# Kernel tuning notes

Measured on AMD Instinct MI355X. Metric: run time of the kernel, lower is better.

Reference implementation:

```python
import jax, jax.numpy as jnp
import numpy as np

N, NFEAT, NHID, NCLASS, NHEAD = 8192, 512, 64, 16, 4
ALPHA = 0.1  # leaky relu slope
NEG = -9e15


def setup_inputs() -> dict:
    key = jax.random.key(0)
    ks = jax.random.split(key, 7)
    x = jax.random.normal(ks[0], (N, NFEAT), dtype=jnp.float32)
    adj = (jax.random.uniform(ks[1], (N, N)) < 0.05).astype(jnp.float32)
    # per-head params: W [H, nfeat, nhid], a [H, 2*nhid] (xavier-ish scale)
    W = jax.random.normal(ks[2], (NHEAD, NFEAT, NHID), dtype=jnp.float32) * (1.0 / np.sqrt(NFEAT))
    a = jax.random.normal(ks[3], (NHEAD, 2 * NHID), dtype=jnp.float32) * (1.0 / np.sqrt(NHID))
    W_out = jax.random.normal(ks[4], (NHEAD * NHID, NCLASS), dtype=jnp.float32) * (1.0 / np.sqrt(NHEAD * NHID))
    a_out = jax.random.normal(ks[5], (2 * NCLASS,), dtype=jnp.float32) * (1.0 / np.sqrt(NCLASS))
    return {"x": x, "adj": adj, "W": W, "a": a, "W_out": W_out, "a_out": a_out}


def _gat_layer(h, adj, Wk, ak):
    """Dense pyGAT GraphAttentionLayer (eval mode, dropout = identity)."""
    d = Wk.shape[1]
    Wh = h @ Wk                         # [N, d]
    f1 = Wh @ ak[:d]                    # [N]
    f2 = Wh @ ak[d:]                    # [N]
    e = jax.nn.leaky_relu(f1[:, None] + f2[None, :], negative_slope=ALPHA)  # [N, N]
    att = jax.nn.softmax(jnp.where(adj > 0, e, NEG), axis=1)
    return att @ Wh                     # [N, d]


def reference(x, adj, W, a, W_out, a_out):
    # eval mode: F.dropout is identity
    heads = jax.vmap(lambda Wk, ak: jax.nn.elu(_gat_layer(x, adj, Wk, ak)))(W, a)  # [H, N, nhid]
    h = jnp.transpose(heads, (1, 0, 2)).reshape(x.shape[0], -1)                    # [N, H*nhid]
    out = jax.nn.elu(_gat_layer(h, adj, W_out, a_out))                             # [N, nclass]
    return jax.nn.log_softmax(out, axis=1)
```

## Files before the change

### kernel.cpp

```cpp
#include <hip/hip_runtime.h>
#include <hip/hip_bf16.h>

#define NN 8192
#define NFEAT 512
#define NHID 64
#define NCLASS 16
#define NHEAD 4
#define ALPHA 0.1f
#define CAP 768
#define ZSPLIT 4
#define JPB (NN / ZSPLIT)
#define DCH 512

typedef short bf16x8 __attribute__((ext_vector_type(8)));
typedef float f32x4 __attribute__((ext_vector_type(4)));
typedef float fv4 __attribute__((ext_vector_type(4)));

__device__ __forceinline__ float lrelu(float x) { return fmaxf(x, ALPHA * x); }
__device__ __forceinline__ float elu(float x) { return x > 0.f ? x : __expf(x) - 1.f; }
__device__ __forceinline__ short f2b(float x) {
  union { __bf16 b; short s; } c; c.b = (__bf16)x; return c.s;
}
__device__ __forceinline__ float b2f(short x) {
  union { unsigned int u; float f; } c; c.u = ((unsigned int)(unsigned short)x) << 16; return c.f;
}

#define UPF(w, v, A0, A1)                                  \
  {                                                        \
    const float lo_ = __uint_as_float((v) << 16);          \
    const float hi_ = __uint_as_float((v) & 0xffff0000u);  \
    (A0) += (w) * lo_;                                     \
    (A1) += (w) * hi_;                                     \
  }

__global__ __launch_bounds__(256) void k_wprep(const float* __restrict__ W,
                                               short* __restrict__ WB) {
  __shared__ float t[64][65];
  const int h = blockIdx.y;
  const int k0 = blockIdx.x * 64;
  const int tid = threadIdx.x;
#pragma unroll
  for (int it = 0; it < 16; ++it) {
    const int r = it * 4 + (tid >> 6), c = tid & 63;
    t[r][c] = W[((size_t)h * NFEAT + k0 + r) * NHID + c];
  }
  __syncthreads();
#pragma unroll
  for (int it = 0; it < 16; ++it) {
    const int d = it * 4 + (tid >> 6), k = tid & 63;
    WB[((size_t)h * NHID + d) * NFEAT + k0 + k] = f2b(t[k][d]);
  }
}

__global__ __launch_bounds__(256) void k_prep1(const float* __restrict__ x,
                                               const short* __restrict__ WB,
                                               const float* __restrict__ a,
                                               short* __restrict__ Whf,
                                               float* __restrict__ f1i,
                                               float* __restrict__ f2i) {
  __shared__ short tile[64][72];
  const int bid = blockIdx.x;
  const int h = bid >> 7;
  const int bm = (bid & 127) * 64;
  const int tid = threadIdx.x;
  const int wv = tid >> 6, lane = tid & 63;
  const int mr = lane & 15, kg = lane >> 4;
  f32x4 acc0 = {0.f, 0.f, 0.f, 0.f}, acc1 = acc0, acc2 = acc0, acc3 = acc0;
  const float* ap = x + (size_t)(bm + wv * 16 + mr) * NFEAT + kg * 8;
  const short* bp = WB + ((size_t)h * NHID + mr) * NFEAT + kg * 8;
#pragma unroll 2
  for (int k0 = 0; k0 < NFEAT; k0 += 32) {
    const float4 xa = *reinterpret_cast<const float4*>(ap);
    const float4 xb = *reinterpret_cast<const float4*>(ap + 4);
    bf16x8 af;
    af[0] = f2b(xa.x); af[1] = f2b(xa.y); af[2] = f2b(xa.z); af[3] = f2b(xa.w);
    af[4] = f2b(xb.x); af[5] = f2b(xb.y); af[6] = f2b(xb.z); af[7] = f2b(xb.w);
    const bf16x8 b0 = *reinterpret_cast<const bf16x8*>(bp);
    const bf16x8 b1 = *reinterpret_cast<const bf16x8*>(bp + 16 * NFEAT);
    const bf16x8 b2 = *reinterpret_cast<const bf16x8*>(bp + 32 * NFEAT);
    const bf16x8 b3 = *reinterpret_cast<const bf16x8*>(bp + 48 * NFEAT);
    acc0 = __builtin_amdgcn_mfma_f32_16x16x32_bf16(af, b0, acc0, 0, 0, 0);
    acc1 = __builtin_amdgcn_mfma_f32_16x16x32_bf16(af, b1, acc1, 0, 0, 0);
    acc2 = __builtin_amdgcn_mfma_f32_16x16x32_bf16(af, b2, acc2, 0, 0, 0);
    acc3 = __builtin_amdgcn_mfma_f32_16x16x32_bf16(af, b3, acc3, 0, 0, 0);
    ap += 32; bp += 32;
  }
  float a1v[4], a2v[4];
#pragma unroll
  for (int c = 0; c < 4; ++c) {
    a1v[c] = a[h * 128 + mr + c * 16];
    a2v[c] = a[h * 128 + 64 + mr + c * 16];
  }
#pragma unroll
  for (int q = 0; q < 4; ++q) {
    float s1 = acc0[q] * a1v[0] + acc1[q] * a1v[1] + acc2[q] * a1v[2] + acc3[q] * a1v[3];
    float s2 = acc0[q] * a2v[0] + acc1[q] * a2v[1] + acc2[q] * a2v[2] + acc3[q] * a2v[3];
#pragma unroll
    for (int off = 1; off < 16; off <<= 1) {
      s1 += __shfl_xor(s1, off);
      s2 += __shfl_xor(s2, off);
    }
    if (mr == 0) {
      const int i = bm + wv * 16 + kg * 4 + q;
      f1i[(size_t)i * 4 + h] = s1;
      f2i[(size_t)i * 4 + h] = s2;
    }
  }
#pragma unroll
  for (int q = 0; q < 4; ++q) {
    const int r = wv * 16 + kg * 4 + q;
    tile[r][mr +  0] = f2b(acc0[q]);
    tile[r][mr + 16] = f2b(acc1[q]);
    tile[r][mr + 32] = f2b(acc2[q]);
    tile[r][mr + 48] = f2b(acc3[q]);
  }
  __syncthreads();
#pragma unroll
  for (int it = 0; it < 2; ++it) {
    const int jbl = (tid >> 6) + it * 4;
    const int d = tid & 63;
    bf16x8 o;
#pragma unroll
    for (int jo = 0; jo < 8; ++jo) o[jo] = tile[jbl * 8 + jo][d];
    *reinterpret_cast<bf16x8*>(Whf +
        (((size_t)h * 1024 + (bm >> 3) + jbl) * 64 + d) * 8) = o;
  }
}

__global__ __launch_bounds__(256) void k_rmax(const float* __restrict__ src,
                                              float* __restrict__ dst, int n, int stride,
                                              int boff) {
  const float* p = src + (size_t)blockIdx.x * boff;
  float m = -1e30f;
  for (int k = threadIdx.x; k < n; k += 256) m = fmaxf(m, p[(size_t)k * stride]);
#pragma unroll
  for (int off = 32; off; off >>= 1) m = fmaxf(m, __shfl_xor(m, off));
  __shared__ float sm[4];
  if ((threadIdx.x & 63) == 0) sm[threadIdx.x >> 6] = m;
  __syncthreads();
  if (threadIdx.x == 0) dst[blockIdx.x] = fmaxf(fmaxf(sm[0], sm[1]), fmaxf(sm[2], sm[3]));
}

__global__ __launch_bounds__(256) void k_acbd(const float* __restrict__ f1i,
                                              const float* __restrict__ f2i,
                                              const float* __restrict__ f2max,
                                              float2* __restrict__ ACh,
                                              unsigned int* __restrict__ BDh) {
  const int idx = blockIdx.x * 256 + threadIdx.x;
  const int i = idx & (NN - 1);
  const int h = idx >> 13;
  const float fm = f2max[h];
  const float f1 = f1i[(size_t)i * 4 + h];
  const float f2 = f2i[(size_t)i * 4 + h];
  const float s = f1 + fm;
  const float mrow = fmaxf(s, 0.1f * s);
  float2 ac;
  ac.x = __expf(s - mrow);
  ac.y = __expf(0.1f * s - mrow);
  ACh[(size_t)h * NN + i] = ac;
  const float t = f2 - fm;
  const unsigned int B = (unsigned short)f2b(__expf(t));
  const unsigned int D = (unsigned short)f2b(__expf(0.1f * t));
  BDh[(size_t)h * NN + i] = B | (D << 16);
}

__global__ __launch_bounds__(256) void k_scan(const float* __restrict__ adj,
                                              unsigned int* __restrict__ bmask) {
  const fv4* a4 = reinterpret_cast<const fv4*>(adj);
  const int t0 = blockIdx.x * 256 + threadIdx.x;
#pragma unroll 4
  for (int it = 0; it < 32; ++it) {
    const int g = it * 524288 + t0;
    const fv4 v = __builtin_nontemporal_load(a4 + g);
    unsigned int nv = (unsigned int)((v.x > 0.f) | ((v.y > 0.f) << 1) |
                                     ((v.z > 0.f) << 2) | ((v.w > 0.f) << 3))
                      << ((threadIdx.x & 7) * 4);
    nv |= __shfl_xor(nv, 1);
    nv |= __shfl_xor(nv, 2);
    nv |= __shfl_xor(nv, 4);
    if ((threadIdx.x & 7) == 0) bmask[g >> 3] = nv;
  }
}

__global__ __launch_bounds__(256) void k_dense1z(const unsigned int* __restrict__ bmask,
                                                 const short* __restrict__ Whf,
                                                 const float2* __restrict__ ACh,
                                                 const unsigned int* __restrict__ BDh,
                                                 float* __restrict__ OpP,
                                                 float* __restrict__ rsP) {
  __shared__ unsigned int sm_mask[64][16];
  __shared__ unsigned int sm_bd[DCH];
  const int i0 = blockIdx.x * 64;
  const int h = blockIdx.y;
  const int z = blockIdx.z;
  const int jb0 = z * JPB;
  const int tid = threadIdx.x;
  const int wv = tid >> 6, lane = tid & 63;
  const int mr = lane & 15, kg = lane >> 4;
  const int row_local = wv * 16 + mr;
  const float2 ac = ACh[(size_t)h * NN + i0 + row_local];
  f32x4 acc0 = {0.f, 0.f, 0.f, 0.f}, acc1 = acc0, acc2 = acc0, acc3 = acc0;
  float rs = 0.f;
  const int rr = tid >> 2, w0 = (tid & 3) * 4;

  for (int jc = jb0; jc < jb0 + JPB; jc += DCH) {
    __syncthreads();
    {
      const unsigned int* src = bmask + (size_t)(i0 + rr) * 256 + (jc >> 5);
#pragma unroll
      for (int u = 0; u < 4; ++u) sm_mask[rr][w0 + u] = src[w0 + u];
      sm_bd[tid] = BDh[(size_t)h * NN + jc + tid];
      sm_bd[tid + 256] = BDh[(size_t)h * NN + jc + tid + 256];
    }
    __syncthreads();
#pragma unroll 4
    for (int ks = 0; ks < DCH / 32; ++ks) {
      const int jl = ks * 32 + kg * 8;
      const uint4 bda = *reinterpret_cast<const uint4*>(&sm_bd[jl]);
      const uint4 bdb = *reinterpret_cast<const uint4*>(&sm_bd[jl + 4]);
      const unsigned int mb = (sm_mask[row_local][ks] >> (kg * 8)) & 0xffu;
      bf16x8 af;
#define MKW(e, bdw)                                              \
      {                                                          \
        const float Bf = __uint_as_float((bdw) << 16);           \
        const float Df = __uint_as_float((bdw) & 0xffff0000u);   \
        float w_ = fmaxf(ac.x * Bf, ac.y * Df);                  \
        w_ = ((mb >> (e)) & 1u) ? w_ : 0.f;                      \
        rs += w_;                                                \
        af[e] = f2b(w_);                                         \
      }
      MKW(0, bda.x) MKW(1, bda.y) MKW(2, bda.z) MKW(3, bda.w)
      MKW(4, bdb.x) MKW(5, bdb.y) MKW(6, bdb.z) MKW(7, bdb.w)
#undef MKW
      const short* wp = Whf + (((size_t)h * 1024 + ((jc + jl) >> 3)) * 64 + mr) * 8;
      const bf16x8 bf0 = *reinterpret_cast<const bf16x8*>(wp);
      const bf16x8 bf1 = *reinterpret_cast<const bf16x8*>(wp + 128);
      const bf16x8 bf2 = *reinterpret_cast<const bf16x8*>(wp + 256);
      const bf16x8 bf3 = *reinterpret_cast<const bf16x8*>(wp + 384);
      acc0 = __builtin_amdgcn_mfma_f32_16x16x32_bf16(af, bf0, acc0, 0, 0, 0);
      acc1 = __builtin_amdgcn_mfma_f32_16x16x32_bf16(af, bf1, acc1, 0, 0, 0);
      acc2 = __builtin_amdgcn_mfma_f32_16x16x32_bf16(af, bf2, acc2, 0, 0, 0);
      acc3 = __builtin_amdgcn_mfma_f32_16x16x32_bf16(af, bf3, acc3, 0, 0, 0);
    }
  }
  rs += __shfl_xor(rs, 16);
  rs += __shfl_xor(rs, 32);
  if (lane < 16)
    rsP[((size_t)z * NHEAD + h) * NN + i0 + wv * 16 + lane] = rs;
  float* op = OpP + (((size_t)z * NHEAD + h) * NN + i0) * 64;
#pragma unroll
  for (int q = 0; q < 4; ++q) {
    const int r = wv * 16 + kg * 4 + q;
    op[(size_t)r * 64 + mr +  0] = acc0[q];
    op[(size_t)r * 64 + mr + 16] = acc1[q];
    op[(size_t)r * 64 + mr + 32] = acc2[q];
    op[(size_t)r * 64 + mr + 48] = acc3[q];
  }
}

__global__ __launch_bounds__(256) void k_comb1(const float* __restrict__ OpP,
                                               const float* __restrict__ rsP,
                                               short* __restrict__ hcat) {
  const int idx = blockIdx.x * 256 + threadIdx.x;
  const int i = idx >> 8;
  const int hc = idx & 255;
  const int h = hc >> 6, d = hc & 63;
  float s = 0.f, rsum = 0.f;
#pragma unroll
  for (int z = 0; z < ZSPLIT; ++z) {
    s += OpP[(((size_t)z * NHEAD + h) * NN + i) * 64 + d];
    rsum += rsP[((size_t)z * NHEAD + h) * NN + i];
  }
  hcat[idx] = f2b(elu(s / rsum));
}

__global__ __launch_bounds__(256) void k_gemm2(const short* __restrict__ hcat,
                                               const float* __restrict__ Wout,
                                               const float* __restrict__ aout,
                                               short* __restrict__ Wh2B,
                                               float* __restrict__ f1o,
                                               float* __restrict__ f2o) {
  __shared__ float sW[NHEAD * NHID][NCLASS + 1];
  __shared__ float sh[16][NHEAD * NHID + 1];
  const int tid = threadIdx.x;
  const int r = tid >> 4, c = tid & 15;
  const int row = blockIdx.x * 16 + r;
  for (int u = tid; u < 256 * 16; u += 256) sW[u >> 4][u & 15] = Wout[u];
  for (int u = tid; u < 16 * 256; u += 256)
    sh[u >> 8][u & 255] = b2f(hcat[(size_t)(blockIdx.x * 16 + (u >> 8)) * 256 + (u & 255)]);
  __syncthreads();
  float acc = 0.f;
#pragma unroll 8
  for (int f = 0; f < 256; ++f) acc += sh[r][f] * sW[f][c];
  Wh2B[(size_t)row * NCLASS + c] = f2b(acc);
  float s1 = acc * aout[c];
  float s2 = acc * aout[NCLASS + c];
#pragma unroll
  for (int off = 8; off; off >>= 1) { s1 += __shfl_xor(s1, off); s2 += __shfl_xor(s2, off); }
  if (c == 0) { f1o[row] = s1; f2o[row] = s2; }
}

__global__ __launch_bounds__(256) void k_attn2(const unsigned int* __restrict__ bmask,
                                               const short* __restrict__ Wh2B,
                                               const float* __restrict__ f1o,
                                               const float* __restrict__ f2o,
                                               const float* __restrict__ f2omax,
                                               float* __restrict__ out) {
  __shared__ unsigned short idx[CAP];
  __shared__ unsigned int wj[CAP + 4];
  __shared__ float red[4][NCLASS];
  __shared__ float swp[4];
  __shared__ float sinvs;
  __shared__ int cnt;
  const int i = blockIdx.x;
  const int tid = threadIdx.x;
  const int wv = tid >> 6, lane = tid & 63;
  if (tid == 0) cnt = 0;
  __syncthreads();

  {
    unsigned int word = bmask[(size_t)i * 256 + tid];
    const int c = __popc(word);
    if (c) {
      int base = atomicAdd(&cnt, c);
      const int j0 = tid * 32;
      while (word) {
        const int b = __ffs(word) - 1;
        word &= word - 1;
        if (base < CAP) idx[base++] = (unsigned short)(j0 + b);
      }
    }
  }
  __syncthreads();
  const int n = min(cnt, CAP);
  if (tid < 4) wj[n + tid] = 0;

  const float f1r = f1o[i];
  const float mrow = lrelu(f1r + f2omax[0]);
  float sw = 0.f;
  for (int k = tid; k < n; k += 256) {
    const int j = idx[k];
    const float w = __expf(lrelu(f1r + f2o[j]) - mrow);
    wj[k] = ((unsigned int)(unsigned short)f2b(w) << 16) | (unsigned int)j;
    sw += w;
  }
#pragma unroll
  for (int off = 32; off; off >>= 1) sw += __shfl_xor(sw, off);
  if (lane == 0) swp[wv] = sw;
  __syncthreads();
  if (tid == 0) sinvs = 1.f / (swp[0] + swp[1] + swp[2] + swp[3]);
  __syncthreads();

  const int grp = tid >> 2, gl = tid & 3;
  float acc0 = 0.f, acc1 = 0.f, acc2 = 0.f, acc3 = 0.f;
  const short* wb = Wh2B + gl * 4;
  for (int kb = grp * 4; kb < n; kb += 256) {
    const uint4 pw = *reinterpret_cast<const uint4*>(wj + kb);
    const uint2 e0 = *reinterpret_cast<const uint2*>(wb + (size_t)(pw.x & 0xffffu) * NCLASS);
    const uint2 e1 = *reinterpret_cast<const uint2*>(wb + (size_t)(pw.y & 0xffffu) * NCLASS);
    const uint2 e2 = *reinterpret_cast<const uint2*>(wb + (size_t)(pw.z & 0xffffu) * NCLASS);
    const uint2 e3 = *reinterpret_cast<const uint2*>(wb + (size_t)(pw.w & 0xffffu) * NCLASS);
    const float w0 = __uint_as_float(pw.x & 0xffff0000u);
    const float w1 = __uint_as_float(pw.y & 0xffff0000u);
    const float w2 = __uint_as_float(pw.z & 0xffff0000u);
    const float w3 = __uint_as_float(pw.w & 0xffff0000u);
    UPF(w0, e0.x, acc0, acc1) UPF(w0, e0.y, acc2, acc3)
    UPF(w1, e1.x, acc0, acc1) UPF(w1, e1.y, acc2, acc3)
    UPF(w2, e2.x, acc0, acc1) UPF(w2, e2.y, acc2, acc3)
    UPF(w3, e3.x, acc0, acc1) UPF(w3, e3.y, acc2, acc3)
  }
  acc0 += __shfl_xor(acc0, 4);  acc1 += __shfl_xor(acc1, 4);
  acc2 += __shfl_xor(acc2, 4);  acc3 += __shfl_xor(acc3, 4);
  acc0 += __shfl_xor(acc0, 8);  acc1 += __shfl_xor(acc1, 8);
  acc2 += __shfl_xor(acc2, 8);  acc3 += __shfl_xor(acc3, 8);
  acc0 += __shfl_xor(acc0, 16); acc1 += __shfl_xor(acc1, 16);
  acc2 += __shfl_xor(acc2, 16); acc3 += __shfl_xor(acc3, 16);
  acc0 += __shfl_xor(acc0, 32); acc1 += __shfl_xor(acc1, 32);
  acc2 += __shfl_xor(acc2, 32); acc3 += __shfl_xor(acc3, 32);
  if (lane < 4) {
    red[wv][lane * 4 + 0] = acc0;
    red[wv][lane * 4 + 1] = acc1;
    red[wv][lane * 4 + 2] = acc2;
    red[wv][lane * 4 + 3] = acc3;
  }
  __syncthreads();
  if (tid < NCLASS) {
    const float s = red[0][tid] + red[1][tid] + red[2][tid] + red[3][tid];
    const float v = elu(s * sinvs);
    float vm = v;
#pragma unroll
    for (int off = 8; off; off >>= 1) vm = fmaxf(vm, __shfl_xor(vm, off, 16));
    float ex = __expf(v - vm);
#pragma unroll
    for (int off = 8; off; off >>= 1) ex += __shfl_xor(ex, off, 16);
    out[(size_t)i * NCLASS + tid] = v - vm - __logf(ex);
  }
}

extern "C" void kernel_launch(void* const* d_in, const int* in_sizes, int n_in,
                              void* d_out, int out_size, void* d_ws, size_t ws_size,
                              hipStream_t stream) {
  const float* x    = (const float*)d_in[0];
  const float* adj  = (const float*)d_in[1];
  const float* W    = (const float*)d_in[2];
  const float* a    = (const float*)d_in[3];
  const float* Wout = (const float*)d_in[4];
  const float* aout = (const float*)d_in[5];
  float* out = (float*)d_out;
  char* ws = (char*)d_ws;
  const size_t MB = 1048576;
  const size_t KB = 1024;

  unsigned int* bmask  = (unsigned int*)(ws);
  short* Whf           = (short*)(ws + 8 * MB);
  short* hcat          = (short*)(ws + 12 * MB);
  float* OpP           = (float*)(ws + 16 * MB);
  float* rsP           = (float*)(ws + 48 * MB);
  short* WB            = (short*)(ws + 49 * MB);
  float* f1i           = (float*)(ws + 49 * MB + 256 * KB);
  float* f2i           = (float*)(ws + 49 * MB + 384 * KB);
  float2* ACh          = (float2*)(ws + 49 * MB + 512 * KB);
  unsigned int* BDh    = (unsigned int*)(ws + 49 * MB + 768 * KB);
  float* f1o           = (float*)(ws + 49 * MB + 896 * KB);
  float* f2o           = (float*)(ws + 49 * MB + 928 * KB);
  short* Wh2B          = (short*)(ws + 49 * MB + 960 * KB);
  float* f2max         = (float*)(ws + 49 * MB + 1216 * KB);
  float* f2omax        = (float*)(ws + 49 * MB + 1216 * KB + 64);

  k_wprep<<<dim3(8, 4), 256, 0, stream>>>(W, WB);
  k_prep1<<<512, 256, 0, stream>>>(x, WB, a, Whf, f1i, f2i);
  k_rmax<<<NHEAD, 256, 0, stream>>>(f2i, f2max, NN, 4, 1);
  k_acbd<<<NN * NHEAD / 256, 256, 0, stream>>>(f1i, f2i, f2max, ACh, BDh);
  k_scan<<<2048, 256, 0, stream>>>(adj, bmask);
  k_dense1z<<<dim3(NN / 64, NHEAD, ZSPLIT), 256, 0, stream>>>(bmask, Whf, ACh, BDh, OpP, rsP);
  k_comb1<<<NN, 256, 0, stream>>>(OpP, rsP, hcat);
  k_gemm2<<<NN / 16, 256, 0, stream>>>(hcat, Wout, aout, Wh2B, f1o, f2o);
  k_rmax<<<1, 256, 0, stream>>>(f2o, f2omax, NN, 1, 0);
  k_attn2<<<NN, 256, 0, stream>>>(bmask, Wh2B, f1o, f2o, f2omax, out);
}
```

Baseline: 226.7 us.

## Fuse adjacency bitmask scan into layer-1 attention kernel with per-wave heads

```diff
diff --git a/kernel.cpp b/kernel.cpp
--- a/kernel.cpp
+++ b/kernel.cpp
@@ -8,9 +8,8 @@
 #define NHEAD 4
 #define ALPHA 0.1f
 #define CAP 768
-#define ZSPLIT 4
+#define ZSPLIT 8
 #define JPB (NN / ZSPLIT)
-#define DCH 512
 
 typedef short bf16x8 __attribute__((ext_vector_type(8)));
 typedef float f32x4 __attribute__((ext_vector_type(4)));
@@ -164,98 +163,120 @@
   BDh[(size_t)h * NN + i] = B | (D << 16);
 }
 
-__global__ __launch_bounds__(256) void k_scan(const float* __restrict__ adj,
-                                              unsigned int* __restrict__ bmask) {
-  const fv4* a4 = reinterpret_cast<const fv4*>(adj);
-  const int t0 = blockIdx.x * 256 + threadIdx.x;
-#pragma unroll 4
-  for (int it = 0; it < 32; ++it) {
-    const int g = it * 524288 + t0;
-    const fv4 v = __builtin_nontemporal_load(a4 + g);
-    unsigned int nv = (unsigned int)((v.x > 0.f) | ((v.y > 0.f) << 1) |
-                                     ((v.z > 0.f) << 2) | ((v.w > 0.f) << 3))
-                      << ((threadIdx.x & 7) * 4);
-    nv |= __shfl_xor(nv, 1);
-    nv |= __shfl_xor(nv, 2);
-    nv |= __shfl_xor(nv, 4);
-    if ((threadIdx.x & 7) == 0) bmask[g >> 3] = nv;
-  }
-}
-
-__global__ __launch_bounds__(256) void k_dense1z(const unsigned int* __restrict__ bmask,
-                                                 const short* __restrict__ Whf,
-                                                 const float2* __restrict__ ACh,
-                                                 const unsigned int* __restrict__ BDh,
-                                                 float* __restrict__ OpP,
-                                                 float* __restrict__ rsP) {
-  __shared__ unsigned int sm_mask[64][16];
-  __shared__ unsigned int sm_bd[DCH];
+__global__ __launch_bounds__(256) void k_fuse1(const float* __restrict__ adj,
+                                               const short* __restrict__ Whf,
+                                               const float2* __restrict__ ACh,
+                                               const unsigned int* __restrict__ BDh,
+                                               float* __restrict__ OpP,
+                                               float* __restrict__ rsP,
+                                               unsigned int* __restrict__ bmask) {
+  __shared__ unsigned int sm_mask[64][33];
   const int i0 = blockIdx.x * 64;
-  const int h = blockIdx.y;
-  const int z = blockIdx.z;
+  const int z = blockIdx.y;
   const int jb0 = z * JPB;
   const int tid = threadIdx.x;
+
+  {
+    const int rr = tid >> 7;
+    const int ct = tid & 127;
+#pragma unroll 2
+    for (int p = 0; p < 32; ++p) {
+      const int row = p * 2 + rr;
+      const fv4* rp = reinterpret_cast<const fv4*>(adj + (size_t)(i0 + row) * NN + jb0) + ct * 2;
+      const fv4 v0 = __builtin_nontemporal_load(rp);
+      const fv4 v1 = __builtin_nontemporal_load(rp + 1);
+      unsigned int b = (unsigned int)(v0.x > 0.f) | ((unsigned int)(v0.y > 0.f) << 1) |
+                       ((unsigned int)(v0.z > 0.f) << 2) | ((unsigned int)(v0.w > 0.f) << 3) |
+                       ((unsigned int)(v1.x > 0.f) << 4) | ((unsigned int)(v1.y > 0.f) << 5) |
+                       ((unsigned int)(v1.z > 0.f) << 6) | ((unsigned int)(v1.w > 0.f) << 7);
+      unsigned int nv = b << ((tid & 3) * 8);
+      nv |= __shfl_xor(nv, 1);
+      nv |= __shfl_xor(nv, 2);
+      if ((tid & 3) == 0) {
+        const int wd = ct >> 2;
+        sm_mask[row][wd] = nv;
+        bmask[(size_t)(i0 + row) * 256 + (jb0 >> 5) + wd] = nv;
+      }
+    }
+  }
+  __syncthreads();
+
   const int wv = tid >> 6, lane = tid & 63;
   const int mr = lane & 15, kg = lane >> 4;
-  const int row_local = wv * 16 + mr;
-  const float2 ac = ACh[(size_t)h * NN + i0 + row_local];
-  f32x4 acc0 = {0.f, 0.f, 0.f, 0.f}, acc1 = acc0, acc2 = acc0, acc3 = acc0;
-  float rs = 0.f;
-  const int rr = tid >> 2, w0 = (tid & 3) * 4;
-
-  for (int jc = jb0; jc < jb0 + JPB; jc += DCH) {
-    __syncthreads();
-    {
-      const unsigned int* src = bmask + (size_t)(i0 + rr) * 256 + (jc >> 5);
-#pragma unroll
-      for (int u = 0; u < 4; ++u) sm_mask[rr][w0 + u] = src[w0 + u];
-      sm_bd[tid] = BDh[(size_t)h * NN + jc + tid];
-      sm_bd[tid + 256] = BDh[(size_t)h * NN + jc + tid + 256];
-    }
-    __syncthreads();
-#pragma unroll 4
-    for (int ks = 0; ks < DCH / 32; ++ks) {
-      const int jl = ks * 32 + kg * 8;
-      const uint4 bda = *reinterpret_cast<const uint4*>(&sm_bd[jl]);
-      const uint4 bdb = *reinterpret_cast<const uint4*>(&sm_bd[jl + 4]);
-      const unsigned int mb = (sm_mask[row_local][ks] >> (kg * 8)) & 0xffu;
-      bf16x8 af;
-#define MKW(e, bdw)                                              \
-      {                                                          \
-        const float Bf = __uint_as_float((bdw) << 16);           \
-        const float Df = __uint_as_float((bdw) & 0xffff0000u);   \
-        float w_ = fmaxf(ac.x * Bf, ac.y * Df);                  \
-        w_ = ((mb >> (e)) & 1u) ? w_ : 0.f;                      \
-        rs += w_;                                                \
-        af[e] = f2b(w_);                                         \
-      }
-      MKW(0, bda.x) MKW(1, bda.y) MKW(2, bda.z) MKW(3, bda.w)
-      MKW(4, bdb.x) MKW(5, bdb.y) MKW(6, bdb.z) MKW(7, bdb.w)
+  const int h = wv;
+  float2 ac0 = ACh[(size_t)h * NN + i0 +  0 + mr];
+  float2 ac1 = ACh[(size_t)h * NN + i0 + 16 + mr];
+  float2 ac2 = ACh[(size_t)h * NN + i0 + 32 + mr];
+  float2 ac3 = ACh[(size_t)h * NN + i0 + 48 + mr];
+  f32x4 acc[4][4];
+#pragma unroll
+  for (int mt = 0; mt < 4; ++mt)
+#pragma unroll
+    for (int dq = 0; dq < 4; ++dq) acc[mt][dq] = (f32x4){0.f, 0.f, 0.f, 0.f};
+  float rs0 = 0.f, rs1 = 0.f, rs2 = 0.f, rs3 = 0.f;
+  const unsigned int* bdh = BDh + (size_t)h * NN + jb0;
+  const short* whb = Whf + ((size_t)h * 1024 + (jb0 >> 3)) * 512 + mr * 8;
+
+  for (int ks = 0; ks < 32; ++ks) {
+    const int jl = ks * 32 + kg * 8;
+    const uint4 bda = *reinterpret_cast<const uint4*>(bdh + jl);
+    const uint4 bdb = *reinterpret_cast<const uint4*>(bdh + jl + 4);
+    const short* wp = whb + (size_t)(jl >> 3) * 512;
+    const bf16x8 bf0 = *reinterpret_cast<const bf16x8*>(wp);
+    const bf16x8 bf1 = *reinterpret_cast<const bf16x8*>(wp + 128);
+    const bf16x8 bf2 = *reinterpret_cast<const bf16x8*>(wp + 256);
+    const bf16x8 bf3 = *reinterpret_cast<const bf16x8*>(wp + 384);
+#define MKW(e, bdw, acv, rsv)                                    \
+    {                                                            \
+      const float Bf = __uint_as_float((bdw) << 16);             \
+      const float Df = __uint_as_float((bdw) & 0xffff0000u);     \
+      float w_ = fmaxf((acv).x * Bf, (acv).y * Df);              \
+      w_ = ((mb >> (e)) & 1u) ? w_ : 0.f;                        \
+      (rsv) += w_;                                               \
+      af[e] = f2b(w_);                                           \
+    }
+#define DOMT(mt, acv, rsv)                                                        \
+    {                                                                             \
+      const unsigned int mb = (sm_mask[(mt) * 16 + mr][ks] >> (kg * 8)) & 0xffu;  \
+      bf16x8 af;                                                                  \
+      MKW(0, bda.x, acv, rsv) MKW(1, bda.y, acv, rsv)                             \
+      MKW(2, bda.z, acv, rsv) MKW(3, bda.w, acv, rsv)                             \
+      MKW(4, bdb.x, acv, rsv) MKW(5, bdb.y, acv, rsv)                             \
+      MKW(6, bdb.z, acv, rsv) MKW(7, bdb.w, acv, rsv)                             \
+      acc[mt][0] = __builtin_amdgcn_mfma_f32_16x16x32_bf16(af, bf0, acc[mt][0], 0, 0, 0); \
+      acc[mt][1] = __builtin_amdgcn_mfma_f32_16x16x32_bf16(af, bf1, acc[mt][1], 0, 0, 0); \
+      acc[mt][2] = __builtin_amdgcn_mfma_f32_16x16x32_bf16(af, bf2, acc[mt][2], 0, 0, 0); \
+      acc[mt][3] = __builtin_amdgcn_mfma_f32_16x16x32_bf16(af, bf3, acc[mt][3], 0, 0, 0); \
+    }
+    DOMT(0, ac0, rs0)
+    DOMT(1, ac1, rs1)
+    DOMT(2, ac2, rs2)
+    DOMT(3, ac3, rs3)
+#undef DOMT
 #undef MKW
-      const short* wp = Whf + (((size_t)h * 1024 + ((jc + jl) >> 3)) * 64 + mr) * 8;
-      const bf16x8 bf0 = *reinterpret_cast<const bf16x8*>(wp);
-      const bf16x8 bf1 = *reinterpret_cast<const bf16x8*>(wp + 128);
-      const bf16x8 bf2 = *reinterpret_cast<const bf16x8*>(wp + 256);
-      const bf16x8 bf3 = *reinterpret_cast<const bf16x8*>(wp + 384);
-      acc0 = __builtin_amdgcn_mfma_f32_16x16x32_bf16(af, bf0, acc0, 0, 0, 0);
-      acc1 = __builtin_amdgcn_mfma_f32_16x16x32_bf16(af, bf1, acc1, 0, 0, 0);
-      acc2 = __builtin_amdgcn_mfma_f32_16x16x32_bf16(af, bf2, acc2, 0, 0, 0);
-      acc3 = __builtin_amdgcn_mfma_f32_16x16x32_bf16(af, bf3, acc3, 0, 0, 0);
-    }
-  }
-  rs += __shfl_xor(rs, 16);
-  rs += __shfl_xor(rs, 32);
-  if (lane < 16)
-    rsP[((size_t)z * NHEAD + h) * NN + i0 + wv * 16 + lane] = rs;
+  }
+  rs0 += __shfl_xor(rs0, 16); rs0 += __shfl_xor(rs0, 32);
+  rs1 += __shfl_xor(rs1, 16); rs1 += __shfl_xor(rs1, 32);
+  rs2 += __shfl_xor(rs2, 16); rs2 += __shfl_xor(rs2, 32);
+  rs3 += __shfl_xor(rs3, 16); rs3 += __shfl_xor(rs3, 32);
+  float* rsp = rsP + ((size_t)z * NHEAD + h) * NN + i0;
+  if (lane < 16) {
+    rsp[ 0 + lane] = rs0;
+    rsp[16 + lane] = rs1;
+    rsp[32 + lane] = rs2;
+    rsp[48 + lane] = rs3;
+  }
   float* op = OpP + (((size_t)z * NHEAD + h) * NN + i0) * 64;
 #pragma unroll
-  for (int q = 0; q < 4; ++q) {
-    const int r = wv * 16 + kg * 4 + q;
-    op[(size_t)r * 64 + mr +  0] = acc0[q];
-    op[(size_t)r * 64 + mr + 16] = acc1[q];
-    op[(size_t)r * 64 + mr + 32] = acc2[q];
-    op[(size_t)r * 64 + mr + 48] = acc3[q];
-  }
+  for (int mt = 0; mt < 4; ++mt)
+#pragma unroll
+    for (int q = 0; q < 4; ++q) {
+      const int r = mt * 16 + kg * 4 + q;
+      op[(size_t)r * 64 + mr +  0] = acc[mt][0][q];
+      op[(size_t)r * 64 + mr + 16] = acc[mt][1][q];
+      op[(size_t)r * 64 + mr + 32] = acc[mt][2][q];
+      op[(size_t)r * 64 + mr + 48] = acc[mt][3][q];
+    }
 }
 
 __global__ __launch_bounds__(256) void k_comb1(const float* __restrict__ OpP,
@@ -415,24 +436,23 @@
   short* Whf           = (short*)(ws + 8 * MB);
   short* hcat          = (short*)(ws + 12 * MB);
   float* OpP           = (float*)(ws + 16 * MB);
-  float* rsP           = (float*)(ws + 48 * MB);
-  short* WB            = (short*)(ws + 49 * MB);
-  float* f1i           = (float*)(ws + 49 * MB + 256 * KB);
-  float* f2i           = (float*)(ws + 49 * MB + 384 * KB);
-  float2* ACh          = (float2*)(ws + 49 * MB + 512 * KB);
-  unsigned int* BDh    = (unsigned int*)(ws + 49 * MB + 768 * KB);
-  float* f1o           = (float*)(ws + 49 * MB + 896 * KB);
-  float* f2o           = (float*)(ws + 49 * MB + 928 * KB);
-  short* Wh2B          = (short*)(ws + 49 * MB + 960 * KB);
-  float* f2max         = (float*)(ws + 49 * MB + 1216 * KB);
-  float* f2omax        = (float*)(ws + 49 * MB + 1216 * KB + 64);
+  float* rsP           = (float*)(ws + 80 * MB);
+  short* WB            = (short*)(ws + 81 * MB);
+  float* f1i           = (float*)(ws + 81 * MB + 256 * KB);
+  float* f2i           = (float*)(ws + 81 * MB + 384 * KB);
+  float2* ACh          = (float2*)(ws + 81 * MB + 512 * KB);
+  unsigned int* BDh    = (unsigned int*)(ws + 81 * MB + 768 * KB);
+  float* f1o           = (float*)(ws + 81 * MB + 896 * KB);
+  float* f2o           = (float*)(ws + 81 * MB + 928 * KB);
+  short* Wh2B          = (short*)(ws + 81 * MB + 960 * KB);
+  float* f2max         = (float*)(ws + 81 * MB + 1216 * KB);
+  float* f2omax        = (float*)(ws + 81 * MB + 1216 * KB + 64);
 
   k_wprep<<<dim3(8, 4), 256, 0, stream>>>(W, WB);
   k_prep1<<<512, 256, 0, stream>>>(x, WB, a, Whf, f1i, f2i);
   k_rmax<<<NHEAD, 256, 0, stream>>>(f2i, f2max, NN, 4, 1);
   k_acbd<<<NN * NHEAD / 256, 256, 0, stream>>>(f1i, f2i, f2max, ACh, BDh);
-  k_scan<<<2048, 256, 0, stream>>>(adj, bmask);
-  k_dense1z<<<dim3(NN / 64, NHEAD, ZSPLIT), 256, 0, stream>>>(bmask, Whf, ACh, BDh, OpP, rsP);
+  k_fuse1<<<dim3(NN / 64, ZSPLIT), 256, 0, stream>>>(adj, Whf, ACh, BDh, OpP, rsP, bmask);
   k_comb1<<<NN, 256, 0, stream>>>(OpP, rsP, hcat);
   k_gemm2<<<NN / 16, 256, 0, stream>>>(hcat, Wout, aout, Wh2B, f1o, f2o);
   k_rmax<<<1, 256, 0, stream>>>(f2o, f2omax, NN, 1, 0);
```

New measurement: 222.8 us. About the same (-1.7%).
